# Kernel optimization log

Measured on AMD Instinct MI355X. Metric: run time of the kernel, lower is better.

Reference implementation:

```python
import jax, jax.numpy as jnp
import numpy as np

D_MODEL = 1024
NUM_HEADS = 16
D_K = D_MODEL // NUM_HEADS


def setup_inputs() -> dict:
    key = jax.random.key(0)
    ks = jax.random.split(key, 8)
    B, S = 2, 2048
    query = jax.random.normal(ks[0], (B, S, D_MODEL), dtype=jnp.float32)
    key_t = jax.random.normal(ks[1], (B, S, D_MODEL), dtype=jnp.float32)
    value = jax.random.normal(ks[2], (B, S, D_MODEL), dtype=jnp.float32)
    # Xavier-uniform projection weights, stored torch-style [out, in]
    lim = float(np.sqrt(6.0 / (D_MODEL + D_MODEL)))
    w_q = jax.random.uniform(ks[3], (D_MODEL, D_MODEL), jnp.float32, -lim, lim)
    w_k = jax.random.uniform(ks[4], (D_MODEL, D_MODEL), jnp.float32, -lim, lim)
    w_v = jax.random.uniform(ks[5], (D_MODEL, D_MODEL), jnp.float32, -lim, lim)
    w_o = jax.random.uniform(ks[6], (D_MODEL, D_MODEL), jnp.float32, -lim, lim)
    b_o = jnp.zeros((D_MODEL,), jnp.float32)
    return {"query": query, "key": key_t, "value": value,
            "w_q": w_q, "w_k": w_k, "w_v": w_v, "w_o": w_o, "b_o": b_o}


def reference(query, key, value, w_q, w_k, w_v, w_o, b_o):
    B, S, _ = query.shape
    H, Dk = NUM_HEADS, D_K
    # Linear projections (torch Linear: x @ W^T), split into heads -> [B,H,S,Dk]
    def proj(x, w):
        return (x @ w.T).reshape(B, S, H, Dk).transpose(0, 2, 1, 3)
    Q = proj(query, w_q)
    K = proj(key, w_k)
    V = proj(value, w_v)
    # Naive attention: materialized [B,H,S,S] scores, softmax, then AV
    scores = jnp.einsum('bhqd,bhkd->bhqk', Q, K) / jnp.sqrt(jnp.float32(Dk))
    attn = jax.nn.softmax(scores, axis=-1)  # dropout is identity in eval mode
    out = jnp.einsum('bhqk,bhkd->bhqd', attn, V)
    out = out.transpose(0, 2, 1, 3).reshape(B, S, H * Dk)
    return out @ w_o.T + b_o
```

## Files before the change

kernel.cpp:

```cpp
#include <hip/hip_runtime.h>
#include <hip/hip_bf16.h>
#include <cstdint>

#define NHEAD 16
#define DKK 64
#define BB 2
#define SS 2048
#define DMODEL 1024

typedef __attribute__((ext_vector_type(8))) short s16x8;
typedef __attribute__((ext_vector_type(4))) float f32x4;
typedef __attribute__((ext_vector_type(4))) int i32x4;

#if __has_builtin(__builtin_amdgcn_exp2f)
#define EXP2(x) __builtin_amdgcn_exp2f(x)
#else
#define EXP2(x) exp2f(x)
#endif

__device__ __forceinline__ void split1(float x, short& h, short& l) {
  __hip_bfloat16 hb = __float2bfloat16(x);
  float hf = __bfloat162float(hb);
  __hip_bfloat16 lb = __float2bfloat16(x - hf);
  h = *reinterpret_cast<short*>(&hb);
  l = *reinterpret_cast<short*>(&lb);
}

__device__ __forceinline__ short bf16s(float x) {
  __hip_bfloat16 b = __float2bfloat16(x);
  return *reinterpret_cast<short*>(&b);
}

__device__ __forceinline__ int pack_trunc(float a, float b) {
  unsigned ua = __builtin_bit_cast(unsigned, a);
  unsigned ub = __builtin_bit_cast(unsigned, b);
  return (int)((ub & 0xFFFF0000u) | (ua >> 16));
}

__device__ __forceinline__ void gl16(const short* g, short* l) {
  __builtin_amdgcn_global_load_lds(
      (const __attribute__((address_space(1))) void*)g,
      (__attribute__((address_space(3))) void*)l, 16, 0, 0);
}

__global__ __launch_bounds__(256) void prep_all(
    const float* __restrict__ w0, const float* __restrict__ w1,
    const float* __restrict__ w2, const float* __restrict__ w3,
    const float* __restrict__ q, const float* __restrict__ k,
    const float* __restrict__ v, short* __restrict__ whi,
    short* __restrict__ wlo, short* __restrict__ xa, short* __restrict__ xb,
    short* __restrict__ xc) {
  const int bid = blockIdx.x;
  if (bid < 4096) {
    const int which = bid >> 10;
    const int i = ((bid & 1023) << 8) + threadIdx.x;
    const float* src = (which == 0) ? w0 : (which == 1) ? w1 : (which == 2) ? w2 : w3;
    float4 vv = ((const float4*)src)[i];
    const size_t hoff = (size_t)which * (DMODEL * DMODEL) + (size_t)i * 4;
    if (which >= 2) {
      short4 h, l;
      split1(vv.x, h.x, l.x);
      split1(vv.y, h.y, l.y);
      split1(vv.z, h.z, l.z);
      split1(vv.w, h.w, l.w);
      *(short4*)&whi[hoff] = h;
      *(short4*)&wlo[(size_t)(which - 2) * (DMODEL * DMODEL) + (size_t)i * 4] = l;
    } else {
      short4 h;
      h.x = bf16s(vv.x); h.y = bf16s(vv.y); h.z = bf16s(vv.z); h.w = bf16s(vv.w);
      *(short4*)&whi[hoff] = h;
    }
  } else {
    const int b2 = bid - 4096;
    const int which = b2 >> 12;
    const int i = ((b2 & 4095) << 8) + threadIdx.x;
    const float* src = (which == 0) ? q : (which == 1) ? k : v;
    short* dst = (which == 0) ? xa : (which == 1) ? xb : xc;
    float4 vv = ((const float4*)src)[i];
    short4 h;
    h.x = bf16s(vv.x); h.y = bf16s(vv.y); h.z = bf16s(vv.z); h.w = bf16s(vv.w);
    *(short4*)&dst[i * 4] = h;
  }
}

__global__ __launch_bounds__(256) void gemm_qkv(
    const short* __restrict__ Xa, const short* __restrict__ Xb,
    const short* __restrict__ Xc, const short* __restrict__ WhiA,
    const short* __restrict__ WloA, float qscale, short* __restrict__ Qb,
    short* __restrict__ Kb, short* __restrict__ Vth) {
  __shared__ short Ah[128 * 64];
  __shared__ short Bhs[128 * 64];
  __shared__ short Bls[128 * 64];

  const int z = blockIdx.z;
  const size_t wsz = (size_t)DMODEL * DMODEL;
  const short* A = (z == 0) ? Xa : (z == 1) ? Xb : Xc;
  const short* Bhi = WhiA + (size_t)z * wsz;
  const short* Blo = WloA;

  const int tid = threadIdx.x;
  const int lane = tid & 63;
  const int w = tid >> 6;
  const int wm = (w >> 1) * 64;
  const int wn = (w & 1) * 64;

  const int flat = blockIdx.y * 8 + blockIdx.x;
  const int f2 = (flat & 7) * 32 + (flat >> 3);
  const int n0 = (f2 & 7) * 128;
  const int m0 = (f2 >> 3) * 128;

  const int srow = lane >> 3;
  const int gslot = (lane & 7) ^ srow;

  f32x4 acc[4][4];
#pragma unroll
  for (int r = 0; r < 4; ++r)
#pragma unroll
    for (int c = 0; c < 4; ++c) acc[r][c] = (f32x4){0.f, 0.f, 0.f, 0.f};

  for (int k0 = 0; k0 < DMODEL; k0 += 64) {
    __syncthreads();
#pragma unroll
    for (int i = 0; i < 4; ++i) {
      const int gb = w * 4 + i;
      const int row = gb * 8 + srow;
      gl16(&A[(size_t)(m0 + row) * DMODEL + k0 + gslot * 8], &Ah[gb * 512]);
      const size_t go = (size_t)(n0 + row) * DMODEL + k0 + gslot * 8;
      gl16(&Bhi[go], &Bhs[gb * 512]);
      if (z == 2) gl16(&Blo[go], &Bls[gb * 512]);
    }
    __syncthreads();

#pragma unroll
    for (int ks = 0; ks < 2; ++ks) {
      const int kslot = (lane >> 4) + ks * 4;
      s16x8 ah[4], bh[4], bl[4];
#pragma unroll
      for (int r = 0; r < 4; ++r) {
        const int row = wm + r * 16 + (lane & 15);
        ah[r] = *(const s16x8*)&Ah[row * 64 + (kslot ^ (row & 7)) * 8];
      }
#pragma unroll
      for (int c = 0; c < 4; ++c) {
        const int row = wn + c * 16 + (lane & 15);
        const int ssw = (kslot ^ (row & 7)) * 8;
        bh[c] = *(const s16x8*)&Bhs[row * 64 + ssw];
        if (z == 2) bl[c] = *(const s16x8*)&Bls[row * 64 + ssw];
      }
#pragma unroll
      for (int r = 0; r < 4; ++r)
#pragma unroll
        for (int c = 0; c < 4; ++c) {
          if (z == 2)
            acc[r][c] = __builtin_amdgcn_mfma_f32_16x16x32_bf16(ah[r], bl[c], acc[r][c], 0, 0, 0);
          acc[r][c] = __builtin_amdgcn_mfma_f32_16x16x32_bf16(ah[r], bh[c], acc[r][c], 0, 0, 0);
        }
    }
  }

  const int lrow = (lane >> 4) * 4;
  const int lcol = lane & 15;
  const float scale = (z == 0) ? qscale : 1.0f;
#pragma unroll
  for (int r = 0; r < 4; ++r)
#pragma unroll
    for (int c = 0; c < 4; ++c) {
      const int n = n0 + wn + c * 16 + lcol;
      const int h = n >> 6;
      const int dk = n & 63;
      if (z < 2) {
        short* Y = (z == 0) ? Qb : Kb;
#pragma unroll
        for (int j = 0; j < 4; ++j) {
          const int m = m0 + wm + r * 16 + lrow + j;
          const size_t off =
              (((size_t)((m >> 11) * NHEAD + h)) * SS + (m & (SS - 1))) * DKK + dk;
          Y[off] = bf16s(acc[r][c][j] * scale);
        }
      } else {
        const int mb = m0 + wm + r * 16 + lrow;
        short4 h4;
        h4.x = bf16s(acc[r][c][0]);
        h4.y = bf16s(acc[r][c][1]);
        h4.z = bf16s(acc[r][c][2]);
        h4.w = bf16s(acc[r][c][3]);
        const size_t off =
            (((size_t)((mb >> 11) * NHEAD + h)) * DKK + dk) * SS + (mb & (SS - 1));
        *(short4*)&Vth[off] = h4;
      }
    }
}

__global__ __launch_bounds__(256) void gemm_split_o(
    const short* __restrict__ Ahi, const short* __restrict__ Alo,
    const short* __restrict__ Bhi, const short* __restrict__ Blo,
    const float* __restrict__ bias, float* __restrict__ Yf) {
  __shared__ short Ah[128 * 64];
  __shared__ short Al[128 * 64];
  __shared__ short Bh[64 * 64];
  __shared__ short Bl[64 * 64];

  const int tid = threadIdx.x;
  const int lane = tid & 63;
  const int w = tid >> 6;
  const int wm = (w >> 1) * 64;
  const int wn = (w & 1) * 32;

  const int flat = blockIdx.y * 16 + blockIdx.x;
  const int f2 = (flat & 7) * 64 + (flat >> 3);
  const int n0 = (f2 & 15) * 64;
  const int m0 = (f2 >> 4) * 128;

  const int srow = lane >> 3;
  const int gslot = (lane & 7) ^ srow;

  f32x4 acc[4][2];
#pragma unroll
  for (int r = 0; r < 4; ++r)
#pragma unroll
    for (int c = 0; c < 2; ++c) acc[r][c] = (f32x4){0.f, 0.f, 0.f, 0.f};

  for (int k0 = 0; k0 < DMODEL; k0 += 64) {
    __syncthreads();
#pragma unroll
    for (int i = 0; i < 4; ++i) {
      const int gb = w * 4 + i;
      const int row = gb * 8 + srow;
      const size_t ga = (size_t)(m0 + row) * DMODEL + k0 + gslot * 8;
      gl16(&Ahi[ga], &Ah[gb * 512]);
      gl16(&Alo[ga], &Al[gb * 512]);
    }
#pragma unroll
    for (int i = 0; i < 2; ++i) {
      const int gb = w * 2 + i;
      const int row = gb * 8 + srow;
      const size_t gbo = (size_t)(n0 + row) * DMODEL + k0 + gslot * 8;
      gl16(&Bhi[gbo], &Bh[gb * 512]);
      gl16(&Blo[gbo], &Bl[gb * 512]);
    }
    __syncthreads();

#pragma unroll
    for (int ks = 0; ks < 2; ++ks) {
      const int kslot = (lane >> 4) + ks * 4;
      s16x8 ah[4], al[4], bh[2], bl[2];
#pragma unroll
      for (int r = 0; r < 4; ++r) {
        const int row = wm + r * 16 + (lane & 15);
        const int ssw = (kslot ^ (row & 7)) * 8;
        ah[r] = *(const s16x8*)&Ah[row * 64 + ssw];
        al[r] = *(const s16x8*)&Al[row * 64 + ssw];
      }
#pragma unroll
      for (int c = 0; c < 2; ++c) {
        const int row = wn + c * 16 + (lane & 15);
        const int ssw = (kslot ^ (row & 7)) * 8;
        bh[c] = *(const s16x8*)&Bh[row * 64 + ssw];
        bl[c] = *(const s16x8*)&Bl[row * 64 + ssw];
      }
#pragma unroll
      for (int r = 0; r < 4; ++r)
#pragma unroll
        for (int c = 0; c < 2; ++c) {
          acc[r][c] = __builtin_amdgcn_mfma_f32_16x16x32_bf16(al[r], bh[c], acc[r][c], 0, 0, 0);
          acc[r][c] = __builtin_amdgcn_mfma_f32_16x16x32_bf16(ah[r], bl[c], acc[r][c], 0, 0, 0);
          acc[r][c] = __builtin_amdgcn_mfma_f32_16x16x32_bf16(ah[r], bh[c], acc[r][c], 0, 0, 0);
        }
    }
  }

  const int lrow = (lane >> 4) * 4;
  const int lcol = lane & 15;
#pragma unroll
  for (int r = 0; r < 4; ++r)
#pragma unroll
    for (int c = 0; c < 2; ++c) {
      const int n = n0 + wn + c * 16 + lcol;
      const float bv = bias[n];
#pragma unroll
      for (int j = 0; j < 4; ++j) {
        const int m = m0 + wm + r * 16 + lrow + j;
        Yf[(size_t)m * DMODEL + n] = acc[r][c][j] + bv;
      }
    }
}

__global__ __launch_bounds__(512) void attn_mfma(
    const short* __restrict__ Qh_g, const short* __restrict__ Kh_g,
    const short* __restrict__ Vh_g,
    short* __restrict__ AOh, short* __restrict__ AOl) {
  __shared__ short Ksh[2][64 * 64];
  __shared__ short Vsh[2][64 * 64];

  const int tid = threadIdx.x;
  const int lane = tid & 63;
  const int w = tid >> 6;
  const int col = lane & 15;
  const int g = lane >> 4;

  const int flat = blockIdx.y * gridDim.x + blockIdx.x;
  const int remap = (flat & 7) * 32 + (flat >> 3);
  const int bh = remap >> 3;
  const int q0 = (remap & 7) * 256;

  const size_t hb = (size_t)bh * SS * DKK;

  const int row0 = tid >> 3;
  const int slot = tid & 7;
  const int kds0 = row0 * 64 + ((slot ^ (row0 & 7)) * 8);
  const int baseA = (slot >> 2) * 8 + ((2 * slot) & 3) * 2 + ((slot >> 1) & 1);
  const int baseB = (slot >> 2) * 8 + ((2 * slot + 1) & 3) * 2 + ((slot >> 1) & 1);
  const int sw0 = (row0 & 7) << 1;
  const int vA0 = row0 * 64 + (baseA ^ sw0) * 4;
  const int vB0 = row0 * 64 + (baseB ^ sw0) * 4;

  s16x8 qbh[2][2];
#pragma unroll
  for (int qq = 0; qq < 2; ++qq)
#pragma unroll
    for (int ks = 0; ks < 2; ++ks) {
      const size_t off =
          hb + (size_t)(q0 + w * 32 + qq * 16 + col) * DKK + g * 8 + ks * 32;
      qbh[qq][ks] = *(const s16x8*)&Qh_g[off];
    }

  f32x4 oacc[2][4];
  f32x4 lacc[2];
#pragma unroll
  for (int qq = 0; qq < 2; ++qq) {
#pragma unroll
    for (int mt = 0; mt < 4; ++mt) oacc[qq][mt] = (f32x4){0.f, 0.f, 0.f, 0.f};
    lacc[qq] = (f32x4){0.f, 0.f, 0.f, 0.f};
  }
  const float SOFF = -12.0f;
  const short ONE = 0x3F80;
  const s16x8 vones = (s16x8){ONE, ONE, ONE, ONE, ONE, ONE, ONE, ONE};

  s16x8 nkh0, nvh0;

#define LOAD_TILE(KV0)                                                        \
  {                                                                           \
    const int kv0_ = (KV0);                                                   \
    nkh0 = *(const s16x8*)&Kh_g[hb + (size_t)(kv0_ + row0) * DKK + slot * 8]; \
    nvh0 = *(const s16x8*)&Vh_g[hb + (size_t)row0 * SS + kv0_ + slot * 8];    \
  }

#define WRITE_TILE(BUF)                                                       \
  {                                                                           \
    *(s16x8*)&Ksh[BUF][kds0] = nkh0;                                          \
    *(short4*)&Vsh[BUF][vA0] = (short4){nvh0[0], nvh0[1], nvh0[2], nvh0[3]};  \
    *(short4*)&Vsh[BUF][vB0] = (short4){nvh0[4], nvh0[5], nvh0[6], nvh0[7]};  \
  }

#define COMPUTE(BUF)                                                          \
  {                                                                           \
    f32x4 sacc[2][4];                                                         \
    _Pragma("unroll") for (int qq = 0; qq < 2; ++qq)                          \
        _Pragma("unroll") for (int mt = 0; mt < 4; ++mt)                      \
            sacc[qq][mt] = (f32x4){SOFF, SOFF, SOFF, SOFF};                   \
    __builtin_amdgcn_s_setprio(1);                                            \
    _Pragma("unroll") for (int mt = 0; mt < 4; ++mt) {                        \
      const int ar = mt * 16 + col;                                           \
      _Pragma("unroll") for (int ks = 0; ks < 2; ++ks) {                      \
        const int as = ar * 64 + (((g + 4 * ks) ^ (ar & 7)) * 8);             \
        const s16x8 kh = *(const s16x8*)&Ksh[BUF][as];                        \
        _Pragma("unroll") for (int qq = 0; qq < 2; ++qq)                      \
            sacc[qq][mt] = __builtin_amdgcn_mfma_f32_16x16x32_bf16(           \
                kh, qbh[qq][ks], sacc[qq][mt], 0, 0, 0);                      \
      }                                                                       \
    }                                                                         \
    __builtin_amdgcn_s_setprio(0);                                            \
    _Pragma("unroll") for (int qq = 0; qq < 2; ++qq)                          \
        _Pragma("unroll") for (int mt = 0; mt < 4; ++mt) {                    \
      sacc[qq][mt][0] = EXP2(sacc[qq][mt][0]);                                \
      sacc[qq][mt][1] = EXP2(sacc[qq][mt][1]);                                \
      sacc[qq][mt][2] = EXP2(sacc[qq][mt][2]);                                \
      sacc[qq][mt][3] = EXP2(sacc[qq][mt][3]);                                \
    }                                                                         \
    s16x8 pbh[2][2];                                                          \
    _Pragma("unroll") for (int qq = 0; qq < 2; ++qq)                          \
        _Pragma("unroll") for (int ks = 0; ks < 2; ++ks) {                    \
      i32x4 pw;                                                               \
      _Pragma("unroll") for (int d = 0; d < 4; ++d) {                         \
        const int mtd = 2 * ks + (d >> 1);                                    \
        const int j0 = (d & 1) * 2;                                           \
        pw[d] = pack_trunc(sacc[qq][mtd][j0], sacc[qq][mtd][j0 + 1]);         \
      }                                                                       \
      pbh[qq][ks] = __builtin_bit_cast(s16x8, pw);                            \
    }                                                                         \
    __builtin_amdgcn_s_setprio(1);                                            \
    _Pragma("unroll") for (int qq = 0; qq < 2; ++qq) {                        \
      lacc[qq] = __builtin_amdgcn_mfma_f32_16x16x32_bf16(                     \
          vones, pbh[qq][0], lacc[qq], 0, 0, 0);                              \
      lacc[qq] = __builtin_amdgcn_mfma_f32_16x16x32_bf16(                     \
          vones, pbh[qq][1], lacc[qq], 0, 0, 0);                              \
    }                                                                         \
    _Pragma("unroll") for (int mt = 0; mt < 4; ++mt) {                        \
      const int row = mt * 16 + col;                                          \
      const int sw = (row & 7) << 1;                                          \
      _Pragma("unroll") for (int ks = 0; ks < 2; ++ks) {                      \
        const int c0 = (8 * ks + 2 * g) ^ sw;                                 \
        const s16x8 vh = *(const s16x8*)&Vsh[BUF][row * 64 + c0 * 4];         \
        _Pragma("unroll") for (int qq = 0; qq < 2; ++qq)                      \
            oacc[qq][mt] = __builtin_amdgcn_mfma_f32_16x16x32_bf16(           \
                vh, pbh[qq][ks], oacc[qq][mt], 0, 0, 0);                      \
      }                                                                       \
    }                                                                         \
    __builtin_amdgcn_s_setprio(0);                                            \
  }

  LOAD_TILE(0);
  WRITE_TILE(0);
  __syncthreads();

  constexpr int NT = SS / 64;
  for (int t = 0; t < NT; t += 2) {
    if (t + 1 < NT) LOAD_TILE((t + 1) * 64);
    COMPUTE(0);
    if (t + 1 < NT) WRITE_TILE(1);
    __syncthreads();
    if (t + 2 < NT) LOAD_TILE((t + 2) * 64);
    COMPUTE(1);
    if (t + 2 < NT) WRITE_TILE(0);
    __syncthreads();
  }

  const int b = bh >> 4;
  const int h = bh & 15;
#pragma unroll
  for (int qq = 0; qq < 2; ++qq) {
    const float inv = 1.0f / lacc[qq][0];
    const int q = q0 + w * 32 + qq * 16 + col;
    const size_t rb = ((size_t)b * SS + q) * DMODEL + h * DKK;
#pragma unroll
    for (int mt = 0; mt < 4; ++mt) {
      short4 h4, l4;
      split1(oacc[qq][mt][0] * inv, h4.x, l4.x);
      split1(oacc[qq][mt][1] * inv, h4.y, l4.y);
      split1(oacc[qq][mt][2] * inv, h4.z, l4.z);
      split1(oacc[qq][mt][3] * inv, h4.w, l4.w);
      *(short4*)&AOh[rb + mt * 16 + g * 4] = h4;
      *(short4*)&AOl[rb + mt * 16 + g * 4] = l4;
    }
  }
#undef LOAD_TILE
#undef WRITE_TILE
#undef COMPUTE
}

extern "C" void kernel_launch(void* const* d_in, const int* in_sizes, int n_in,
                              void* d_out, int out_size, void* d_ws,
                              size_t ws_size, hipStream_t stream) {
  const float* query = (const float*)d_in[0];
  const float* key   = (const float*)d_in[1];
  const float* value = (const float*)d_in[2];
  const float* w_q   = (const float*)d_in[3];
  const float* w_k   = (const float*)d_in[4];
  const float* w_v   = (const float*)d_in[5];
  const float* w_o   = (const float*)d_in[6];
  const float* b_o   = (const float*)d_in[7];
  float* out = (float*)d_out;

  const size_t per = (size_t)BB * NHEAD * SS * DKK;
  const size_t wsz = (size_t)DMODEL * DMODEL;
  short* Qbh = (short*)d_ws;
  short* Kbh = Qbh + per;
  short* Vth = Kbh + per;
  short* Xa  = Vth + per;
  short* Xb  = Xa + per;
  short* Xc  = Xb + per;
  short* WhiA = Xc + per;
  short* WloA = WhiA + 4 * wsz;

  const float QSCALE = 0.125f * 1.4426950408889634f;
  dim3 blk(256);

  prep_all<<<16384, blk, 0, stream>>>(w_q, w_k, w_v, w_o, query, key, value,
                                      WhiA, WloA, Xa, Xb, Xc);

  dim3 gqkv(DMODEL / 128, (BB * SS) / 128, 3);
  gemm_qkv<<<gqkv, blk, 0, stream>>>(Xa, Xb, Xc, WhiA, WloA, QSCALE, Qbh, Kbh,
                                     Vth);

  dim3 gattn(SS / 256, BB * NHEAD);
  attn_mfma<<<gattn, dim3(512), 0, stream>>>(Qbh, Kbh, Vth, Xa, Xb);

  dim3 ggemm(DMODEL / 64, (BB * SS) / 128);
  gemm_split_o<<<ggemm, blk, 0, stream>>>(Xa, Xb, WhiA + 3 * wsz,
                                          WloA + 1 * wsz, b_o, out);
}
```

Baseline: 121.8 us.

## Split KV sequence across two warp groups with LDS reduction of partial outputs

The 512-thread block is split into two 256-thread groups. Each group handles alternating 64-row KV tiles over all 256 queries, so each wave now owns 64 query rows and reuses every K/V LDS fragment for four query sub-tiles instead of two. The partial output accumulators and row sums of group 1 are reduced through LDS into group 0 before normalisation and store. This cuts LDS reads per MFMA and halves the sequential KV iterations per group. The cost is doubled accumulator registers (possible occupancy loss or spills), doubled LDS footprint, and an extra reduction phase at the end.

```diff
diff --git a/kernel.cpp b/kernel.cpp
--- a/kernel.cpp
+++ b/kernel.cpp
@@ -289,12 +289,14 @@
     const short* __restrict__ Qh_g, const short* __restrict__ Kh_g,
     const short* __restrict__ Vh_g,
     short* __restrict__ AOh, short* __restrict__ AOl) {
-  __shared__ short Ksh[2][64 * 64];
-  __shared__ short Vsh[2][64 * 64];
+  __shared__ short lds[2][2][2][64 * 64];
+  __shared__ float Lsh[256];
 
   const int tid = threadIdx.x;
+  const int grp = tid >> 8;
+  const int gtid = tid & 255;
   const int lane = tid & 63;
-  const int w = tid >> 6;
+  const int w = gtid >> 6;
   const int col = lane & 15;
   const int g = lane >> 4;
 
@@ -305,29 +307,32 @@
 
   const size_t hb = (size_t)bh * SS * DKK;
 
-  const int row0 = tid >> 3;
-  const int slot = tid & 7;
+  const int row0 = gtid >> 3, row1 = row0 + 32;
+  const int slot = gtid & 7;
   const int kds0 = row0 * 64 + ((slot ^ (row0 & 7)) * 8);
+  const int kds1 = row1 * 64 + ((slot ^ (row1 & 7)) * 8);
   const int baseA = (slot >> 2) * 8 + ((2 * slot) & 3) * 2 + ((slot >> 1) & 1);
   const int baseB = (slot >> 2) * 8 + ((2 * slot + 1) & 3) * 2 + ((slot >> 1) & 1);
-  const int sw0 = (row0 & 7) << 1;
+  const int sw0 = (row0 & 7) << 1, sw1 = (row1 & 7) << 1;
   const int vA0 = row0 * 64 + (baseA ^ sw0) * 4;
   const int vB0 = row0 * 64 + (baseB ^ sw0) * 4;
-
-  s16x8 qbh[2][2];
-#pragma unroll
-  for (int qq = 0; qq < 2; ++qq)
+  const int vA1 = row1 * 64 + (baseA ^ sw1) * 4;
+  const int vB1 = row1 * 64 + (baseB ^ sw1) * 4;
+
+  s16x8 qbh[4][2];
+#pragma unroll
+  for (int qq = 0; qq < 4; ++qq)
 #pragma unroll
     for (int ks = 0; ks < 2; ++ks) {
       const size_t off =
-          hb + (size_t)(q0 + w * 32 + qq * 16 + col) * DKK + g * 8 + ks * 32;
+          hb + (size_t)(q0 + w * 64 + qq * 16 + col) * DKK + g * 8 + ks * 32;
       qbh[qq][ks] = *(const s16x8*)&Qh_g[off];
     }
 
-  f32x4 oacc[2][4];
-  f32x4 lacc[2];
-#pragma unroll
-  for (int qq = 0; qq < 2; ++qq) {
+  f32x4 oacc[4][4];
+  f32x4 lacc[4];
+#pragma unroll
+  for (int qq = 0; qq < 4; ++qq) {
 #pragma unroll
     for (int mt = 0; mt < 4; ++mt) oacc[qq][mt] = (f32x4){0.f, 0.f, 0.f, 0.f};
     lacc[qq] = (f32x4){0.f, 0.f, 0.f, 0.f};
@@ -336,26 +341,31 @@
   const short ONE = 0x3F80;
   const s16x8 vones = (s16x8){ONE, ONE, ONE, ONE, ONE, ONE, ONE, ONE};
 
-  s16x8 nkh0, nvh0;
+  s16x8 nkh0, nvh0, nkh1, nvh1;
 
 #define LOAD_TILE(KV0)                                                        \
   {                                                                           \
     const int kv0_ = (KV0);                                                   \
     nkh0 = *(const s16x8*)&Kh_g[hb + (size_t)(kv0_ + row0) * DKK + slot * 8]; \
+    nkh1 = *(const s16x8*)&Kh_g[hb + (size_t)(kv0_ + row1) * DKK + slot * 8]; \
     nvh0 = *(const s16x8*)&Vh_g[hb + (size_t)row0 * SS + kv0_ + slot * 8];    \
+    nvh1 = *(const s16x8*)&Vh_g[hb + (size_t)row1 * SS + kv0_ + slot * 8];    \
   }
 
 #define WRITE_TILE(BUF)                                                       \
   {                                                                           \
-    *(s16x8*)&Ksh[BUF][kds0] = nkh0;                                          \
-    *(short4*)&Vsh[BUF][vA0] = (short4){nvh0[0], nvh0[1], nvh0[2], nvh0[3]};  \
-    *(short4*)&Vsh[BUF][vB0] = (short4){nvh0[4], nvh0[5], nvh0[6], nvh0[7]};  \
+    *(s16x8*)&lds[grp][BUF][0][kds0] = nkh0;                                  \
+    *(s16x8*)&lds[grp][BUF][0][kds1] = nkh1;                                  \
+    *(short4*)&lds[grp][BUF][1][vA0] = (short4){nvh0[0], nvh0[1], nvh0[2], nvh0[3]}; \
+    *(short4*)&lds[grp][BUF][1][vB0] = (short4){nvh0[4], nvh0[5], nvh0[6], nvh0[7]}; \
+    *(short4*)&lds[grp][BUF][1][vA1] = (short4){nvh1[0], nvh1[1], nvh1[2], nvh1[3]}; \
+    *(short4*)&lds[grp][BUF][1][vB1] = (short4){nvh1[4], nvh1[5], nvh1[6], nvh1[7]}; \
   }
 
 #define COMPUTE(BUF)                                                          \
   {                                                                           \
-    f32x4 sacc[2][4];                                                         \
-    _Pragma("unroll") for (int qq = 0; qq < 2; ++qq)                          \
+    f32x4 sacc[4][4];                                                         \
+    _Pragma("unroll") for (int qq = 0; qq < 4; ++qq)                          \
         _Pragma("unroll") for (int mt = 0; mt < 4; ++mt)                      \
             sacc[qq][mt] = (f32x4){SOFF, SOFF, SOFF, SOFF};                   \
     __builtin_amdgcn_s_setprio(1);                                            \
@@ -363,22 +373,22 @@
       const int ar = mt * 16 + col;                                           \
       _Pragma("unroll") for (int ks = 0; ks < 2; ++ks) {                      \
         const int as = ar * 64 + (((g + 4 * ks) ^ (ar & 7)) * 8);             \
-        const s16x8 kh = *(const s16x8*)&Ksh[BUF][as];                        \
-        _Pragma("unroll") for (int qq = 0; qq < 2; ++qq)                      \
+        const s16x8 kh = *(const s16x8*)&lds[grp][BUF][0][as];                \
+        _Pragma("unroll") for (int qq = 0; qq < 4; ++qq)                      \
             sacc[qq][mt] = __builtin_amdgcn_mfma_f32_16x16x32_bf16(           \
                 kh, qbh[qq][ks], sacc[qq][mt], 0, 0, 0);                      \
       }                                                                       \
     }                                                                         \
     __builtin_amdgcn_s_setprio(0);                                            \
-    _Pragma("unroll") for (int qq = 0; qq < 2; ++qq)                          \
+    _Pragma("unroll") for (int qq = 0; qq < 4; ++qq)                          \
         _Pragma("unroll") for (int mt = 0; mt < 4; ++mt) {                    \
       sacc[qq][mt][0] = EXP2(sacc[qq][mt][0]);                                \
       sacc[qq][mt][1] = EXP2(sacc[qq][mt][1]);                                \
       sacc[qq][mt][2] = EXP2(sacc[qq][mt][2]);                                \
       sacc[qq][mt][3] = EXP2(sacc[qq][mt][3]);                                \
     }                                                                         \
-    s16x8 pbh[2][2];                                                          \
-    _Pragma("unroll") for (int qq = 0; qq < 2; ++qq)                          \
+    s16x8 pbh[4][2];                                                          \
+    _Pragma("unroll") for (int qq = 0; qq < 4; ++qq)                          \
         _Pragma("unroll") for (int ks = 0; ks < 2; ++ks) {                    \
       i32x4 pw;                                                               \
       _Pragma("unroll") for (int d = 0; d < 4; ++d) {                         \
@@ -389,7 +399,7 @@
       pbh[qq][ks] = __builtin_bit_cast(s16x8, pw);                            \
     }                                                                         \
     __builtin_amdgcn_s_setprio(1);                                            \
-    _Pragma("unroll") for (int qq = 0; qq < 2; ++qq) {                        \
+    _Pragma("unroll") for (int qq = 0; qq < 4; ++qq) {                        \
       lacc[qq] = __builtin_amdgcn_mfma_f32_16x16x32_bf16(                     \
           vones, pbh[qq][0], lacc[qq], 0, 0, 0);                              \
       lacc[qq] = __builtin_amdgcn_mfma_f32_16x16x32_bf16(                     \
@@ -400,8 +410,8 @@
       const int sw = (row & 7) << 1;                                          \
       _Pragma("unroll") for (int ks = 0; ks < 2; ++ks) {                      \
         const int c0 = (8 * ks + 2 * g) ^ sw;                                 \
-        const s16x8 vh = *(const s16x8*)&Vsh[BUF][row * 64 + c0 * 4];         \
-        _Pragma("unroll") for (int qq = 0; qq < 2; ++qq)                      \
+        const s16x8 vh = *(const s16x8*)&lds[grp][BUF][1][row * 64 + c0 * 4]; \
+        _Pragma("unroll") for (int qq = 0; qq < 4; ++qq)                      \
             oacc[qq][mt] = __builtin_amdgcn_mfma_f32_16x16x32_bf16(           \
                 vh, pbh[qq][ks], oacc[qq][mt], 0, 0, 0);                      \
       }                                                                       \
@@ -409,38 +419,56 @@
     __builtin_amdgcn_s_setprio(0);                                            \
   }
 
-  LOAD_TILE(0);
+  LOAD_TILE(64 * grp);
   WRITE_TILE(0);
   __syncthreads();
 
-  constexpr int NT = SS / 64;
-  for (int t = 0; t < NT; t += 2) {
-    if (t + 1 < NT) LOAD_TILE((t + 1) * 64);
+  for (int i = 0; i < 16; i += 2) {
+    if (i + 1 < 16) LOAD_TILE(128 * (i + 1) + 64 * grp);
     COMPUTE(0);
-    if (t + 1 < NT) WRITE_TILE(1);
+    if (i + 1 < 16) WRITE_TILE(1);
     __syncthreads();
-    if (t + 2 < NT) LOAD_TILE((t + 2) * 64);
+    if (i + 2 < 16) LOAD_TILE(128 * (i + 2) + 64 * grp);
     COMPUTE(1);
-    if (t + 2 < NT) WRITE_TILE(0);
+    if (i + 2 < 16) WRITE_TILE(0);
     __syncthreads();
   }
 
-  const int b = bh >> 4;
-  const int h = bh & 15;
-#pragma unroll
-  for (int qq = 0; qq < 2; ++qq) {
-    const float inv = 1.0f / lacc[qq][0];
-    const int q = q0 + w * 32 + qq * 16 + col;
-    const size_t rb = ((size_t)b * SS + q) * DMODEL + h * DKK;
-#pragma unroll
-    for (int mt = 0; mt < 4; ++mt) {
-      short4 h4, l4;
-      split1(oacc[qq][mt][0] * inv, h4.x, l4.x);
-      split1(oacc[qq][mt][1] * inv, h4.y, l4.y);
-      split1(oacc[qq][mt][2] * inv, h4.z, l4.z);
-      split1(oacc[qq][mt][3] * inv, h4.w, l4.w);
-      *(short4*)&AOh[rb + mt * 16 + g * 4] = h4;
-      *(short4*)&AOl[rb + mt * 16 + g * 4] = l4;
+  float* fbuf = (float*)&lds[0][0][0][0];
+  if (grp == 1) {
+#pragma unroll
+    for (int qq = 0; qq < 4; ++qq) {
+      Lsh[(w * 4 + qq) * 16 + col] = lacc[qq][0];
+#pragma unroll
+      for (int mt = 0; mt < 4; ++mt) {
+        const int idx = ((w * 4 + qq) * 4 + mt) * 256 + lane * 4;
+        *(float4*)&fbuf[idx] = make_float4(oacc[qq][mt][0], oacc[qq][mt][1],
+                                           oacc[qq][mt][2], oacc[qq][mt][3]);
+      }
+    }
+  }
+  __syncthreads();
+  if (grp == 0) {
+    const int b = bh >> 4;
+    const int h = bh & 15;
+#pragma unroll
+    for (int qq = 0; qq < 4; ++qq) {
+      const float l1 = Lsh[(w * 4 + qq) * 16 + col];
+      const float inv = 1.0f / (lacc[qq][0] + l1);
+      const int q = q0 + w * 64 + qq * 16 + col;
+      const size_t rb = ((size_t)b * SS + q) * DMODEL + h * DKK;
+#pragma unroll
+      for (int mt = 0; mt < 4; ++mt) {
+        const int idx = ((w * 4 + qq) * 4 + mt) * 256 + lane * 4;
+        const float4 o1 = *(const float4*)&fbuf[idx];
+        short4 h4, l4;
+        split1((oacc[qq][mt][0] + o1.x) * inv, h4.x, l4.x);
+        split1((oacc[qq][mt][1] + o1.y) * inv, h4.y, l4.y);
+        split1((oacc[qq][mt][2] + o1.z) * inv, h4.z, l4.z);
+        split1((oacc[qq][mt][3] + o1.w) * inv, h4.w, l4.w);
+        *(short4*)&AOh[rb + mt * 16 + g * 4] = h4;
+        *(short4*)&AOl[rb + mt * 16 + g * 4] = l4;
+      }
     }
   }
 #undef LOAD_TILE
```

Result: no change. 120.1 us (-1.4%).
